# Performance work log

Measured on AMD Instinct MI355X. Metric: run time of the kernel, lower is better.

The kernel has to match this reference:

```python
import jax, jax.numpy as jnp
import numpy as np

B, S, H, NH = 4, 2048, 1024, 16
D = H // NH  # head_dim = 64


def setup_inputs() -> dict:
    key = jax.random.key(0)
    ks = jax.random.split(key, 8)
    hidden_states = jax.random.normal(ks[0], (B, S, H), dtype=jnp.float32)
    attention_mask = jnp.zeros((B, 1, 1, S), dtype=jnp.float32)  # additive, bidirectional
    # RoPE tables (cos/sin per position, full head_dim)
    inv_freq = 1.0 / (10000.0 ** (jnp.arange(0, D, 2, dtype=jnp.float32) / D))
    t = jnp.arange(S, dtype=jnp.float32)
    freqs = jnp.outer(t, inv_freq)              # [S, D/2]
    emb = jnp.concatenate([freqs, freqs], -1)   # [S, D]
    cos, sin = jnp.cos(emb), jnp.sin(emb)
    scale = 1.0 / np.sqrt(H)
    Wq = jax.random.normal(ks[1], (H, H), dtype=jnp.float32) * scale
    Wk = jax.random.normal(ks[2], (H, H), dtype=jnp.float32) * scale
    Wv = jax.random.normal(ks[3], (H, H), dtype=jnp.float32) * scale
    Wo = jax.random.normal(ks[4], (H, H), dtype=jnp.float32) * scale
    return {"hidden_states": hidden_states, "attention_mask": attention_mask,
            "cos": cos, "sin": sin, "Wq": Wq, "Wk": Wk, "Wv": Wv, "Wo": Wo}


def _rotate_half(x):
    x1, x2 = jnp.split(x, 2, axis=-1)
    return jnp.concatenate([-x2, x1], axis=-1)


def _rope(x, cos, sin):
    # x: [B, NH, S, D]; cos/sin: [S, D]
    c = cos[None, None, :, :]
    s = sin[None, None, :, :]
    return x * c + _rotate_half(x) * s


def reference(hidden_states, attention_mask, cos, sin, Wq, Wk, Wv, Wo):
    b, s, h = hidden_states.shape
    # QKV projections (torch Linear: x @ W^T)
    def proj(W):
        y = jnp.einsum('bsh,oh->bso', hidden_states, W)
        return y.reshape(b, s, NH, D).transpose(0, 2, 1, 3)  # [B, NH, S, D]
    q, k, v = proj(Wq), proj(Wk), proj(Wv)
    q = _rope(q, cos, sin)
    k = _rope(k, cos, sin)
    scale = D ** -0.5
    scores = jnp.einsum('bhqd,bhkd->bhqk', q, k) * scale + attention_mask
    attn = jax.nn.softmax(scores, axis=-1)
    out = jnp.einsum('bhqk,bhkd->bhqd', attn, v)            # [B, NH, S, D]
    out = out.transpose(0, 2, 1, 3).reshape(b, s, h)        # [B, S, H]
    return jnp.einsum('bsh,oh->bso', out, Wo)
```

## Files before the change

### kernel.cpp

```cpp
#include <hip/hip_runtime.h>


typedef __bf16 bf16x8 __attribute__((ext_vector_type(8)));
typedef float f32x4 __attribute__((ext_vector_type(4)));
typedef unsigned short u16x8 __attribute__((ext_vector_type(8)));
typedef unsigned short u16x4 __attribute__((ext_vector_type(4)));
typedef const __attribute__((address_space(1))) void* gptr_t;
typedef __attribute__((address_space(3))) void* lptr_t;

template <int N> struct ic { static constexpr int v = N; };

__device__ __forceinline__ unsigned short f2bf(float f) {
  union { float f; unsigned u; } v; v.f = f;
  unsigned r = (v.u + 0x7fffu + ((v.u >> 16) & 1u)) >> 16;
  return (unsigned short)r;
}

__device__ __forceinline__ unsigned short f2bfn(float f) {
  union { __bf16 h; unsigned short u; } v;
  v.h = (__bf16)f;
  return v.u;
}

__device__ __forceinline__ void gld16(const void* g, void* l) {
  __builtin_amdgcn_global_load_lds((gptr_t)g, (lptr_t)l, 16, 0, 0);
}

__global__ __launch_bounds__(256) void cvt_all(
    const float* __restrict__ hidden, const float* __restrict__ Wq,
    const float* __restrict__ Wk, const float* __restrict__ Wv,
    const float* __restrict__ Wo, unsigned short* __restrict__ Xb,
    unsigned short* __restrict__ Wb) {
  size_t i8 = ((size_t)blockIdx.x * 256 + threadIdx.x) * 8;
  const float* src;
  unsigned short* dst;
  if (i8 < 8388608) {
    src = hidden + i8;
    dst = Xb + i8;
  } else {
    size_t r = i8 - 8388608;
    int wsel = (int)(r >> 20);
    size_t off = r & 1048575;
    const float* wsrc = (wsel == 0) ? Wq : (wsel == 1) ? Wk : (wsel == 2) ? Wv : Wo;
    src = wsrc + off;
    dst = Wb + r;
  }
  f32x4 a = *(const f32x4*)(src);
  f32x4 b = *(const f32x4*)(src + 4);
  u16x8 o;
  o[0] = f2bf(a[0]); o[1] = f2bf(a[1]); o[2] = f2bf(a[2]); o[3] = f2bf(a[3]);
  o[4] = f2bf(b[0]); o[5] = f2bf(b[1]); o[6] = f2bf(b[2]); o[7] = f2bf(b[3]);
  *(u16x8*)dst = o;
}

__global__ __launch_bounds__(256, 3) void gemm_k(
    const unsigned short* __restrict__ A,
    const unsigned short* __restrict__ W0, const unsigned short* __restrict__ W1,
    const unsigned short* __restrict__ W2,
    const float* __restrict__ cosT, const float* __restrict__ sinT,
    unsigned short* __restrict__ Qh, unsigned short* __restrict__ Kh,
    unsigned short* __restrict__ Vh, float* __restrict__ Cout, int mode) {
  __shared__ char sm[32768];
  char* As = sm;
  char* Bs = sm + 16384;
  const int tid = threadIdx.x, lane = tid & 63, w = tid >> 6;
  const int wm = w >> 1, wn = w & 1;
  const int brow = blockIdx.y * 128;
  const int bcol = blockIdx.x * 128;
  const unsigned short* Wsel =
      (mode == 0) ? W0 : (blockIdx.z == 0 ? W0 : (blockIdx.z == 1 ? W1 : W2));

  f32x4 acc[4][4];
#pragma unroll
  for (int m = 0; m < 4; ++m)
#pragma unroll
    for (int n = 0; n < 4; ++n) acc[m][n] = (f32x4){0.f, 0.f, 0.f, 0.f};

  const char* Abase = (const char*)A + (size_t)brow * 2048;
  const char* Bbase = (const char*)Wsel + (size_t)bcol * 2048;

  for (int kt = 0; kt < 1024; kt += 64) {
#pragma unroll
    for (int c = 0; c < 4; ++c) {
      int Lb = w * 4096 + c * 1024;
      int L = Lb + lane * 16;
      int r = L >> 7, kb = L & 127;
      int sw = kb ^ ((r & 7) << 4);
      gld16(Abase + (size_t)r * 2048 + kt * 2 + sw, As + Lb);
      gld16(Bbase + (size_t)r * 2048 + kt * 2 + sw, Bs + Lb);
    }
    __syncthreads();
#pragma unroll
    for (int kk = 0; kk < 2; ++kk) {
      int kb = kk * 64 + (lane >> 4) * 16;
      bf16x8 af[4], bfr[4];
#pragma unroll
      for (int m = 0; m < 4; ++m) {
        int r = wm * 64 + m * 16 + (lane & 15);
        af[m] = *(const bf16x8*)(As + r * 128 + (kb ^ ((r & 7) << 4)));
      }
#pragma unroll
      for (int n = 0; n < 4; ++n) {
        int r = wn * 64 + n * 16 + (lane & 15);
        bfr[n] = *(const bf16x8*)(Bs + r * 128 + (kb ^ ((r & 7) << 4)));
      }
#pragma unroll
      for (int m = 0; m < 4; ++m)
#pragma unroll
        for (int n = 0; n < 4; ++n)
          acc[m][n] = __builtin_amdgcn_mfma_f32_16x16x32_bf16(af[m], bfr[n],
                                                              acc[m][n], 0, 0, 0);
    }
    __syncthreads();
  }

  if (mode == 0) {
#pragma unroll
    for (int m = 0; m < 4; ++m)
#pragma unroll
      for (int n = 0; n < 4; ++n)
#pragma unroll
        for (int i = 0; i < 4; ++i) {
          int row = brow + wm * 64 + m * 16 + (lane >> 4) * 4 + i;
          int col = bcol + wn * 64 + n * 16 + (lane & 15);
          Cout[(size_t)row * 1024 + col] = acc[m][n][i];
        }
  } else {
    const int z = blockIdx.z;
    const int h = (bcol + wn * 64) >> 6;
    if (z == 2) {
#pragma unroll
      for (int m = 0; m < 4; ++m) {
        int row0 = brow + wm * 64 + m * 16 + (lane >> 4) * 4;
        int b = row0 >> 11, s0 = row0 & 2047;
        size_t base = (size_t)(b * 16 + h) * 64 * 2048 + s0;
#pragma unroll
        for (int n = 0; n < 4; ++n) {
          int dl = n * 16 + (lane & 15);
          u16x4 pw;
#pragma unroll
          for (int i = 0; i < 4; ++i) pw[i] = f2bf(acc[m][n][i]);
          *(u16x4*)(Vh + base + (size_t)dl * 2048) = pw;
        }
      }
    } else {
      unsigned short* dst = (z == 0) ? Qh : Kh;
      const float qs = (z == 0) ? 0.18033688f : 1.0f;
#pragma unroll
      for (int m = 0; m < 4; ++m)
#pragma unroll
        for (int i = 0; i < 4; ++i) {
          int row = brow + wm * 64 + m * 16 + (lane >> 4) * 4 + i;
          int b = row >> 11, s = row & 2047;
          size_t hb2 = ((size_t)(b * 16 + h) * 2048 + s) * 64;
#pragma unroll
          for (int n = 0; n < 2; ++n) {
            int dl = n * 16 + (lane & 15);
            float c = cosT[s * 64 + dl], sn = sinT[s * 64 + dl];
            float lo = acc[m][n][i], hi = acc[m][n + 2][i];
            dst[hb2 + dl] = f2bf((lo * c - hi * sn) * qs);
            dst[hb2 + dl + 32] = f2bf((hi * c + lo * sn) * qs);
          }
        }
    }
  }
}

__global__ __launch_bounds__(256, 4) void attn_k(
    const unsigned short* __restrict__ Q, const unsigned short* __restrict__ K,
    const unsigned short* __restrict__ Vt, const float* __restrict__ mask,
    unsigned short* __restrict__ O) {
  __shared__ char Ks[2][8192];
  __shared__ char Vs[2][8192];
  __shared__ char Ps[4][2048];
  const int tid = threadIdx.x, lane = tid & 63, w = tid >> 6;
  const int l15 = lane & 15, h2 = lane >> 4;
  const int wg = blockIdx.x;
  const int work = (wg & 7) * 256 + (wg >> 3);
  const int qt = work & 31, hl = work >> 5;
  const int h = hl & 15, b = hl >> 4;
  const size_t hb = (size_t)(b * 16 + h) * (2048 * 64);
  const int q0 = qt * 64 + w * 16;
  const float L2E = 1.44269504f;
  const float MREF = 12.0f;
  const int pswz = (l15 & 7) << 4;

  bf16x8 qa0, qa1;
  {
    const char* qrow = (const char*)(Q + hb + (size_t)(q0 + l15) * 64);
    qa0 = *(const bf16x8*)(qrow + h2 * 16);
    qa1 = *(const bf16x8*)(qrow + 64 + h2 * 16);
  }

  float l_part = 0.f;
  f32x4 oacc[4];
#pragma unroll
  for (int n = 0; n < 4; ++n) oacc[n] = (f32x4){0.f, 0.f, 0.f, 0.f};

  int koff0, koff1, vof0, vof1;
  {
    int L0 = w * 2048 + lane * 16, r0 = L0 >> 7, c0 = L0 & 127;
    koff0 = r0 * 128 + (c0 ^ ((r0 & 7) << 4));
    int L1 = L0 + 1024, r1 = L1 >> 7, c1 = L1 & 127;
    koff1 = r1 * 128 + (c1 ^ ((r1 & 7) << 4));
    int d0 = w * 16 + (lane >> 3);
    vof0 = d0 * 4096 + (((lane & 7) * 16) ^ ((d0 & 7) << 4));
    int d1 = d0 + 8;
    vof1 = d1 * 4096 + (((lane & 7) * 16) ^ ((d1 & 7) << 4));
  }
  const char* Kg = (const char*)(K + hb);
  const char* Vg = (const char*)(Vt + hb);
  const float* mp = mask + (size_t)b * 2048;
  char* PsW = Ps[w];

  gld16(Kg + koff0, Ks[0] + w * 2048);
  gld16(Kg + koff1, Ks[0] + w * 2048 + 1024);
  gld16(Vg + vof0, Vs[0] + w * 2048);
  gld16(Vg + vof1, Vs[0] + w * 2048 + 1024);
  __syncthreads();

  auto body = [&](auto curc, int t) {
    constexpr int cur = decltype(curc)::v;
    constexpr int nxt = 1 - cur;
    if (t < 31) {
      const char* kp = Kg + (size_t)(t + 1) * 8192;
      const char* vp = Vg + (size_t)(t + 1) * 128;
      gld16(kp + koff0, Ks[nxt] + w * 2048);
      gld16(kp + koff1, Ks[nxt] + w * 2048 + 1024);
      gld16(vp + vof0, Vs[nxt] + w * 2048);
      gld16(vp + vof1, Vs[nxt] + w * 2048 + 1024);
    }
    const float* mrow = mp + t * 64;
    f32x4 mm[4];
#pragma unroll
    for (int n = 0; n < 4; ++n) {
      f32x4 mv = *(const f32x4*)(mrow + n * 16 + h2 * 4);
#pragma unroll
      for (int i = 0; i < 4; ++i) mm[n][i] = fmaf(mv[i], L2E, -MREF);
    }

    f32x4 sacc[4];
#pragma unroll
    for (int n = 0; n < 4; ++n) sacc[n] = (f32x4){0.f, 0.f, 0.f, 0.f};
    __builtin_amdgcn_s_setprio(1);
#pragma unroll
    for (int kk = 0; kk < 2; ++kk) {
      const int kbb = kk * 64 + h2 * 16;
#pragma unroll
      for (int n = 0; n < 4; ++n) {
        bf16x8 kf =
            *(const bf16x8*)(Ks[cur] + (n * 16 + l15) * 128 + (kbb ^ pswz));
        sacc[n] = __builtin_amdgcn_mfma_f32_16x16x32_bf16(
            kf, kk ? qa1 : qa0, sacc[n], 0, 0, 0);
      }
    }
    __builtin_amdgcn_s_setprio(0);

#pragma unroll
    for (int n = 0; n < 4; ++n)
#pragma unroll
      for (int i = 0; i < 4; ++i)
        sacc[n][i] = __builtin_amdgcn_exp2f(sacc[n][i] + mm[n][i]);
#pragma unroll
    for (int n = 0; n < 4; ++n)
      l_part += (sacc[n][0] + sacc[n][1]) + (sacc[n][2] + sacc[n][3]);
#pragma unroll
    for (int n = 0; n < 4; ++n) {
      u16x4 pw;
#pragma unroll
      for (int i = 0; i < 4; ++i) pw[i] = f2bfn(sacc[n][i]);
      *(u16x4*)(PsW + l15 * 128 + ((n * 32 + h2 * 8) ^ pswz)) = pw;
    }
    asm volatile("s_waitcnt lgkmcnt(0)" ::: "memory");
    __builtin_amdgcn_sched_barrier(0);

    __builtin_amdgcn_s_setprio(1);
#pragma unroll
    for (int kvh = 0; kvh < 2; ++kvh) {
      const int kvb = kvh * 64 + h2 * 16;
      bf16x8 pa = *(const bf16x8*)(PsW + l15 * 128 + (kvb ^ pswz));
#pragma unroll
      for (int n = 0; n < 4; ++n) {
        bf16x8 vf =
            *(const bf16x8*)(Vs[cur] + (n * 16 + l15) * 128 + (kvb ^ pswz));
        oacc[n] = __builtin_amdgcn_mfma_f32_16x16x32_bf16(pa, vf, oacc[n],
                                                          0, 0, 0);
      }
    }
    __builtin_amdgcn_s_setprio(0);
    __syncthreads();
  };

  for (int t = 0; t < 32; t += 2) {
    body(ic<0>{}, t);
    body(ic<1>{}, t + 1);
  }

  float lr = l_part;
  lr += __shfl_xor(lr, 16, 64);
  lr += __shfl_xor(lr, 32, 64);
#pragma unroll
  for (int i = 0; i < 4; ++i) {
    float li = __shfl(lr, h2 * 4 + i, 64);
    float inv = 1.0f / li;
    int row = b * 2048 + q0 + h2 * 4 + i;
    size_t rb = (size_t)row * 1024 + h * 64;
#pragma unroll
    for (int n = 0; n < 4; ++n)
      O[rb + n * 16 + l15] = f2bfn(oacc[n][i] * inv);
  }
}

extern "C" void kernel_launch(void* const* d_in, const int* in_sizes, int n_in,
                              void* d_out, int out_size, void* d_ws, size_t ws_size,
                              hipStream_t stream) {
  const float* hidden = (const float*)d_in[0];
  const float* amask = (const float*)d_in[1];
  const float* cosT = (const float*)d_in[2];
  const float* sinT = (const float*)d_in[3];
  const float* Wq = (const float*)d_in[4];
  const float* Wk = (const float*)d_in[5];
  const float* Wv = (const float*)d_in[6];
  const float* Wo = (const float*)d_in[7];
  float* out = (float*)d_out;

  if (ws_size < (size_t)92274688) return;
  unsigned short* Xb = (unsigned short*)d_ws;
  unsigned short* Wqb = Xb + (size_t)8192 * 1024;
  unsigned short* Wkb = Wqb + (size_t)1024 * 1024;
  unsigned short* Wvb = Wkb + (size_t)1024 * 1024;
  unsigned short* Wob = Wvb + (size_t)1024 * 1024;
  unsigned short* Qh = Wob + (size_t)1024 * 1024;
  unsigned short* Kh = Qh + (size_t)8388608;
  unsigned short* Vt = Kh + (size_t)8388608;
  unsigned short* Ob = Vt + (size_t)8388608;

  cvt_all<<<6144, 256, 0, stream>>>(hidden, Wq, Wk, Wv, Wo, Xb, Wqb);

  gemm_k<<<dim3(8, 64, 3), 256, 0, stream>>>(Xb, Wqb, Wkb, Wvb, cosT, sinT, Qh, Kh,
                                             Vt, nullptr, 1);
  attn_k<<<2048, 256, 0, stream>>>(Qh, Kh, Vt, amask, Ob);
  gemm_k<<<dim3(8, 64, 1), 256, 0, stream>>>(Ob, Wob, Wob, Wob, cosT, sinT, nullptr,
                                             nullptr, nullptr, out, 0);
}
```

Before: 230.4 us.

## Switch attention to 32x32 MFMA with register-resident P via permlane swap

The attention kernel now processes 32 query rows per wave (128 per workgroup) using 32x32x16 bf16 MFMAs instead of 16x16x32. The softmax probabilities stay in registers: they are packed with v_cvt_pk_bf16_f32 and rearranged with v_permlane32_swap into the A-operand layout, which removes the per-wave LDS round trip for P and its waitcnt. K/V tiles are reused across twice as many queries, and the grid is halved. In exchange, register pressure rises from the larger accumulators, and with half as many workgroups there is less occupancy and parallelism across CUs.

```diff
diff --git a/kernel.cpp b/kernel.cpp
--- a/kernel.cpp
+++ b/kernel.cpp
@@ -3,6 +3,7 @@
 
 typedef __bf16 bf16x8 __attribute__((ext_vector_type(8)));
 typedef float f32x4 __attribute__((ext_vector_type(4)));
+typedef float f32x16 __attribute__((ext_vector_type(16)));
 typedef unsigned short u16x8 __attribute__((ext_vector_type(8)));
 typedef unsigned short u16x4 __attribute__((ext_vector_type(4)));
 typedef const __attribute__((address_space(1))) void* gptr_t;
@@ -20,6 +21,12 @@
   union { __bf16 h; unsigned short u; } v;
   v.h = (__bf16)f;
   return v.u;
+}
+
+__device__ __forceinline__ unsigned cvtpk(float lo, float hi_) {
+  unsigned r;
+  asm("v_cvt_pk_bf16_f32 %0, %1, %2" : "=v"(r) : "v"(lo), "v"(hi_));
+  return r;
 }
 
 __device__ __forceinline__ void gld16(const void* g, void* l) {
@@ -172,30 +179,31 @@
     unsigned short* __restrict__ O) {
   __shared__ char Ks[2][8192];
   __shared__ char Vs[2][8192];
-  __shared__ char Ps[4][2048];
+  __shared__ float l_arr[4][32];
   const int tid = threadIdx.x, lane = tid & 63, w = tid >> 6;
-  const int l15 = lane & 15, h2 = lane >> 4;
+  const int q31 = lane & 31, hi = lane >> 5;
   const int wg = blockIdx.x;
-  const int work = (wg & 7) * 256 + (wg >> 3);
-  const int qt = work & 31, hl = work >> 5;
+  const int work = (wg & 7) * 128 + (wg >> 3);
+  const int qt = work & 15, hl = work >> 4;
   const int h = hl & 15, b = hl >> 4;
   const size_t hb = (size_t)(b * 16 + h) * (2048 * 64);
-  const int q0 = qt * 64 + w * 16;
+  const int q0 = qt * 128 + w * 32;
   const float L2E = 1.44269504f;
   const float MREF = 12.0f;
-  const int pswz = (l15 & 7) << 4;
-
-  bf16x8 qa0, qa1;
+  const int kswz = (q31 & 7) << 4;
+
+  bf16x8 qb[4];
   {
-    const char* qrow = (const char*)(Q + hb + (size_t)(q0 + l15) * 64);
-    qa0 = *(const bf16x8*)(qrow + h2 * 16);
-    qa1 = *(const bf16x8*)(qrow + 64 + h2 * 16);
+    const char* qrow = (const char*)(Q + hb + (size_t)(q0 + q31) * 64);
+#pragma unroll
+    for (int ks = 0; ks < 4; ++ks)
+      qb[ks] = *(const bf16x8*)(qrow + ks * 32 + hi * 16);
   }
 
   float l_part = 0.f;
-  f32x4 oacc[4];
-#pragma unroll
-  for (int n = 0; n < 4; ++n) oacc[n] = (f32x4){0.f, 0.f, 0.f, 0.f};
+  f32x16 oacc[2];
+#pragma unroll
+  for (int e = 0; e < 16; ++e) { oacc[0][e] = 0.f; oacc[1][e] = 0.f; }
 
   int koff0, koff1, vof0, vof1;
   {
@@ -211,7 +219,6 @@
   const char* Kg = (const char*)(K + hb);
   const char* Vg = (const char*)(Vt + hb);
   const float* mp = mask + (size_t)b * 2048;
-  char* PsW = Ps[w];
 
   gld16(Kg + koff0, Ks[0] + w * 2048);
   gld16(Kg + koff1, Ks[0] + w * 2048 + 1024);
@@ -231,59 +238,57 @@
       gld16(vp + vof1, Vs[nxt] + w * 2048 + 1024);
     }
     const float* mrow = mp + t * 64;
-    f32x4 mm[4];
-#pragma unroll
-    for (int n = 0; n < 4; ++n) {
-      f32x4 mv = *(const f32x4*)(mrow + n * 16 + h2 * 4);
-#pragma unroll
-      for (int i = 0; i < 4; ++i) mm[n][i] = fmaf(mv[i], L2E, -MREF);
-    }
-
-    f32x4 sacc[4];
-#pragma unroll
-    for (int n = 0; n < 4; ++n) sacc[n] = (f32x4){0.f, 0.f, 0.f, 0.f};
+
+    f32x16 sacc[2];
+#pragma unroll
+    for (int c = 0; c < 2; ++c) {
+#pragma unroll
+      for (int g = 0; g < 4; ++g) {
+        f32x4 mv = *(const f32x4*)(mrow + c * 32 + g * 8 + hi * 4);
+#pragma unroll
+        for (int i = 0; i < 4; ++i)
+          sacc[c][g * 4 + i] = fmaf(mv[i], L2E, -MREF);
+      }
+      __builtin_amdgcn_s_setprio(1);
+#pragma unroll
+      for (int ks = 0; ks < 4; ++ks) {
+        bf16x8 kf = *(const bf16x8*)(Ks[cur] + (c * 32 + q31) * 128 +
+                                     ((ks * 32 + hi * 16) ^ kswz));
+        sacc[c] = __builtin_amdgcn_mfma_f32_32x32x16_bf16(kf, qb[ks], sacc[c],
+                                                          0, 0, 0);
+      }
+      __builtin_amdgcn_s_setprio(0);
+#pragma unroll
+      for (int e = 0; e < 16; ++e)
+        sacc[c][e] = __builtin_amdgcn_exp2f(sacc[c][e]);
+      float s0 = (sacc[c][0] + sacc[c][1]) + (sacc[c][2] + sacc[c][3]);
+      float s1 = (sacc[c][4] + sacc[c][5]) + (sacc[c][6] + sacc[c][7]);
+      float s2 = (sacc[c][8] + sacc[c][9]) + (sacc[c][10] + sacc[c][11]);
+      float s3 = (sacc[c][12] + sacc[c][13]) + (sacc[c][14] + sacc[c][15]);
+      l_part += (s0 + s1) + (s2 + s3);
+    }
+
     __builtin_amdgcn_s_setprio(1);
 #pragma unroll
-    for (int kk = 0; kk < 2; ++kk) {
-      const int kbb = kk * 64 + h2 * 16;
-#pragma unroll
-      for (int n = 0; n < 4; ++n) {
-        bf16x8 kf =
-            *(const bf16x8*)(Ks[cur] + (n * 16 + l15) * 128 + (kbb ^ pswz));
-        sacc[n] = __builtin_amdgcn_mfma_f32_16x16x32_bf16(
-            kf, kk ? qa1 : qa0, sacc[n], 0, 0, 0);
-      }
-    }
-    __builtin_amdgcn_s_setprio(0);
-
-#pragma unroll
-    for (int n = 0; n < 4; ++n)
-#pragma unroll
-      for (int i = 0; i < 4; ++i)
-        sacc[n][i] = __builtin_amdgcn_exp2f(sacc[n][i] + mm[n][i]);
-#pragma unroll
-    for (int n = 0; n < 4; ++n)
-      l_part += (sacc[n][0] + sacc[n][1]) + (sacc[n][2] + sacc[n][3]);
-#pragma unroll
-    for (int n = 0; n < 4; ++n) {
-      u16x4 pw;
-#pragma unroll
-      for (int i = 0; i < 4; ++i) pw[i] = f2bfn(sacc[n][i]);
-      *(u16x4*)(PsW + l15 * 128 + ((n * 32 + h2 * 8) ^ pswz)) = pw;
-    }
-    asm volatile("s_waitcnt lgkmcnt(0)" ::: "memory");
-    __builtin_amdgcn_sched_barrier(0);
-
-    __builtin_amdgcn_s_setprio(1);
-#pragma unroll
-    for (int kvh = 0; kvh < 2; ++kvh) {
-      const int kvb = kvh * 64 + h2 * 16;
-      bf16x8 pa = *(const bf16x8*)(PsW + l15 * 128 + (kvb ^ pswz));
-#pragma unroll
-      for (int n = 0; n < 4; ++n) {
-        bf16x8 vf =
-            *(const bf16x8*)(Vs[cur] + (n * 16 + l15) * 128 + (kvb ^ pswz));
-        oacc[n] = __builtin_amdgcn_mfma_f32_16x16x32_bf16(pa, vf, oacc[n],
+    for (int c = 0; c < 2; ++c) {
+#pragma unroll
+      for (int par = 0; par < 2; ++par) {
+        const int t2 = c * 2 + par;
+        unsigned a0 = cvtpk(sacc[c][par * 8 + 0], sacc[c][par * 8 + 1]);
+        unsigned a1 = cvtpk(sacc[c][par * 8 + 2], sacc[c][par * 8 + 3]);
+        unsigned b0 = cvtpk(sacc[c][par * 8 + 4], sacc[c][par * 8 + 5]);
+        unsigned b1 = cvtpk(sacc[c][par * 8 + 6], sacc[c][par * 8 + 7]);
+        asm("v_permlane32_swap_b32 %0, %1" : "+v"(a0), "+v"(b0));
+        asm("v_permlane32_swap_b32 %0, %1" : "+v"(a1), "+v"(b1));
+        union { unsigned u[4]; bf16x8 v; } pu;
+        pu.u[0] = a0; pu.u[1] = a1; pu.u[2] = b0; pu.u[3] = b1;
+        bf16x8 vf0 = *(const bf16x8*)(Vs[cur] + q31 * 128 +
+                                      ((t2 * 32 + hi * 16) ^ kswz));
+        bf16x8 vf1 = *(const bf16x8*)(Vs[cur] + (32 + q31) * 128 +
+                                      ((t2 * 32 + hi * 16) ^ kswz));
+        oacc[0] = __builtin_amdgcn_mfma_f32_32x32x16_bf16(pu.v, vf0, oacc[0],
+                                                          0, 0, 0);
+        oacc[1] = __builtin_amdgcn_mfma_f32_32x32x16_bf16(pu.v, vf1, oacc[1],
                                                           0, 0, 0);
       }
     }
@@ -296,18 +301,19 @@
     body(ic<1>{}, t + 1);
   }
 
-  float lr = l_part;
-  lr += __shfl_xor(lr, 16, 64);
-  lr += __shfl_xor(lr, 32, 64);
-#pragma unroll
-  for (int i = 0; i < 4; ++i) {
-    float li = __shfl(lr, h2 * 4 + i, 64);
-    float inv = 1.0f / li;
-    int row = b * 2048 + q0 + h2 * 4 + i;
-    size_t rb = (size_t)row * 1024 + h * 64;
-#pragma unroll
-    for (int n = 0; n < 4; ++n)
-      O[rb + n * 16 + l15] = f2bfn(oacc[n][i] * inv);
+  float lr = l_part + __shfl_xor(l_part, 32, 64);
+  l_arr[w][q31] = 1.0f / lr;
+
+#pragma unroll
+  for (int g = 0; g < 4; ++g) {
+    f32x4 iv = *(const f32x4*)(&l_arr[w][g * 8 + hi * 4]);
+    const int qrow = q0 + g * 8 + hi * 4;
+#pragma unroll
+    for (int i = 0; i < 4; ++i) {
+      size_t rb = (size_t)(b * 2048 + qrow + i) * 1024 + h * 64;
+      O[rb + q31] = f2bfn(oacc[0][g * 4 + i] * iv[i]);
+      O[rb + 32 + q31] = f2bfn(oacc[1][g * 4 + i] * iv[i]);
+    }
   }
 }
 
@@ -339,7 +345,7 @@
 
   gemm_k<<<dim3(8, 64, 3), 256, 0, stream>>>(Xb, Wqb, Wkb, Wvb, cosT, sinT, Qh, Kh,
                                              Vt, nullptr, 1);
-  attn_k<<<2048, 256, 0, stream>>>(Qh, Kh, Vt, amask, Ob);
+  attn_k<<<1024, 256, 0, stream>>>(Qh, Kh, Vt, amask, Ob);
   gemm_k<<<dim3(8, 64, 1), 256, 0, stream>>>(Ob, Wob, Wob, Wob, cosT, sinT, nullptr,
                                              nullptr, nullptr, out, 0);
 }
```

Measured after the change: 214.4 us. 1.07x faster.
